# Performance work log

Measured on AMD Instinct MI355X. Metric: run time of the kernel, lower is better.

Reference implementation:

```python
import jax, jax.numpy as jnp
from jax import lax
import numpy as np

K = 7          # kernel size
PAD = 3        # (K-1)//2
KK = K * K     # 49 taps


def setup_inputs() -> dict:
    key = jax.random.key(0)
    ks = jax.random.split(key, 5)
    B, C, H, W = 8, 256, 128, 128
    x = jax.random.normal(ks[0], (B, C, H, W), jnp.float32)
    # conv_offset: Conv2d(2, 3*KK, k=7, pad=3). Small init so offsets are modest.
    w_off = jax.random.normal(ks[1], (3 * KK, 2, K, K), jnp.float32) * 0.01
    b_off = jax.random.normal(ks[2], (3 * KK,), jnp.float32) * 0.01
    # DCN weight: Conv2d(2, 1, k=7)
    w_dcn = jax.random.normal(ks[3], (1, 2, K, K), jnp.float32) * (1.0 / np.sqrt(2 * KK))
    b_dcn = jnp.zeros((1,), jnp.float32)
    bn_gamma = jnp.ones((1,), jnp.float32)
    bn_beta = jnp.zeros((1,), jnp.float32)
    bn_mean = jnp.zeros((1,), jnp.float32)
    bn_var = jnp.ones((1,), jnp.float32)
    return {"x": x, "w_off": w_off, "b_off": b_off, "w_dcn": w_dcn,
            "b_dcn": b_dcn, "bn_gamma": bn_gamma, "bn_beta": bn_beta,
            "bn_mean": bn_mean, "bn_var": bn_var}


def _deform_spatial_att(x, w_off, b_off, w_dcn, b_dcn, bn_gamma, bn_beta, bn_mean, bn_var):
    B, C, H, W = x.shape
    dt = x.dtype
    # channel mean / max pooling -> [B, 2, H, W]
    y = jnp.concatenate([x.mean(1, keepdims=True), x.max(1, keepdims=True)], axis=1)

    # offset/mask generator conv (mmcv ModulatedDeformConv2dPack.conv_offset)
    off = lax.conv_general_dilated(y, w_off, (1, 1), [(PAD, PAD), (PAD, PAD)])
    off = off + b_off[None, :, None, None]                     # [B, 3*KK, H, W]
    o1, o2, m = off[:, :KK], off[:, KK:2 * KK], off[:, 2 * KK:]
    offset = jnp.concatenate([o1, o2], axis=1)                 # [B, 2*KK, H, W]
    dy = offset[:, 0::2]                                       # y-offset per tap, [B, KK, H, W]
    dx = offset[:, 1::2]                                       # x-offset per tap
    mask = jax.nn.sigmoid(m)                                   # modulation, [B, KK, H, W]

    # sampling locations: p = p0 + p_k + offset
    kk = jnp.arange(K, dtype=dt) - PAD
    ky = jnp.repeat(kk, K)                                     # [KK]
    kx = jnp.tile(kk, K)                                       # [KK]
    hh = jnp.arange(H, dtype=dt)
    ww = jnp.arange(W, dtype=dt)
    py = hh[None, None, :, None] + ky[None, :, None, None] + dy   # [B, KK, H, W]
    px = ww[None, None, None, :] + kx[None, :, None, None] + dx

    # bilinear sampling with zero padding outside the feature map
    y0 = jnp.floor(py)
    x0 = jnp.floor(px)
    iy0 = y0.astype(jnp.int32)
    ix0 = x0.astype(jnp.int32)
    iy1 = iy0 + 1
    ix1 = ix0 + 1
    wy1 = py - y0
    wy0 = 1.0 - wy1
    wx1 = px - x0
    wx0 = 1.0 - wx1

    y_flat = y.reshape(B, 2, H * W)

    def gather(iy, ix):
        valid = ((iy >= 0) & (iy < H) & (ix >= 0) & (ix < W))
        idx = jnp.clip(iy, 0, H - 1) * W + jnp.clip(ix, 0, W - 1)   # [B, KK, H, W]
        g = jax.vmap(lambda yb, ib: yb[:, ib])(y_flat, idx)          # [B, 2, KK, H, W]
        return g * valid[:, None].astype(dt)

    val = (gather(iy0, ix0) * (wy0 * wx0)[:, None]
           + gather(iy0, ix1) * (wy0 * wx1)[:, None]
           + gather(iy1, ix0) * (wy1 * wx0)[:, None]
           + gather(iy1, ix1) * (wy1 * wx1)[:, None])                # [B, 2, KK, H, W]

    sampled = val * mask[:, None]
    # deformable conv accumulation: 2 in-channels x 49 taps -> 1 out-channel
    out = jnp.einsum('bckhw,ck->bhw', sampled, w_dcn[0].reshape(2, KK)) + b_dcn
    out = out[:, None]                                               # [B, 1, H, W]

    # BatchNorm2d(1), inference-mode normalization
    eps = 1e-5
    out = (out - bn_mean[None, :, None, None]) * (bn_gamma[None, :, None, None]
          * lax.rsqrt(bn_var[None, :, None, None] + eps)) + bn_beta[None, :, None, None]

    gate = jax.nn.sigmoid(out)                                       # [B, 1, H, W]
    return jnp.broadcast_to(gate, x.shape)


def reference(x, w_off, b_off, w_dcn, b_dcn, bn_gamma, bn_beta, bn_mean, bn_var):
    return _deform_spatial_att(x, w_off, b_off, w_dcn, b_dcn,
                               bn_gamma, bn_beta, bn_mean, bn_var)
```

## Files before the change

kernel.cpp:

```cpp
#include <hip/hip_runtime.h>
#include <cstdint>

#define BB 8
#define CC 256
#define HH 128
#define WW 128
#define HW (HH * WW)

typedef __attribute__((ext_vector_type(8))) short bf16x8;
typedef __attribute__((ext_vector_type(4))) float f32x4;

__device__ __forceinline__ uint32_t f2bf(float f) {
    uint32_t u = __float_as_uint(f);
    return (u + 0x7FFFu + ((u >> 16) & 1u)) >> 16;
}
__device__ __forceinline__ float bf2f(uint32_t u) {
    return __uint_as_float(u << 16);
}

__global__ __launch_bounds__(512) void reduce_meanmax(const float* __restrict__ x,
                                                      float* __restrict__ y2,
                                                      const float* __restrict__ w_off,
                                                      uint16_t* __restrict__ Bpre) {
    const int bh = blockIdx.x;
    const int b  = bh >> 7;
    const int h  = bh & 127;
    const int t  = threadIdx.x;

    if (t < 20) {
        const int idx = bh * 20 + t;
        const int e   = idx & 7;
        const int t1  = idx >> 3;
        const int j   = t1 % 160;
        const int grp = t1 / 160;
        uint16_t v = 0;
        if (grp < 14 && e < 7 && j < 147) {
            const int ci = grp / 7, r = grp % 7;
            const int ch = (j < 49) ? (2 * j) : ((j < 98) ? (2 * (j - 49) + 1) : j);
            v = (uint16_t)f2bf(w_off[(size_t)ch * 98 + ci * 49 + r * 7 + e]);
        }
        Bpre[idx] = v;
    }

    const int wq = t & 31;
    const int cg = t >> 5;
    const float* xb = x + ((size_t)(b * CC + cg * 16) * HH + h) * WW;

    float4 s = make_float4(0.f, 0.f, 0.f, 0.f);
    float4 m = make_float4(-INFINITY, -INFINITY, -INFINITY, -INFINITY);
    #pragma unroll 4
    for (int i = 0; i < 16; ++i) {
        float4 v = ((const float4*)(xb + (size_t)i * HW))[wq];
        s.x += v.x; s.y += v.y; s.z += v.z; s.w += v.w;
        m.x = fmaxf(m.x, v.x); m.y = fmaxf(m.y, v.y);
        m.z = fmaxf(m.z, v.z); m.w = fmaxf(m.w, v.w);
    }

    __shared__ float4 ls[16][32];
    __shared__ float4 lm[16][32];
    ls[cg][wq] = s;
    lm[cg][wq] = m;
    __syncthreads();

    if (t < 32) {
        float4 S = ls[0][t];
        float4 M = lm[0][t];
        #pragma unroll
        for (int g = 1; g < 16; ++g) {
            float4 a = ls[g][t];
            float4 c = lm[g][t];
            S.x += a.x; S.y += a.y; S.z += a.z; S.w += a.w;
            M.x = fmaxf(M.x, c.x); M.y = fmaxf(M.y, c.y);
            M.z = fmaxf(M.z, c.z); M.w = fmaxf(M.w, c.w);
        }
        const float inv = 1.0f / 256.0f;
        float4 o0 = make_float4(S.x * inv, M.x, S.y * inv, M.y);
        float4 o1 = make_float4(S.z * inv, M.z, S.w * inv, M.w);
        float4* yo = (float4*)(y2 + ((size_t)b * HW + (size_t)h * WW) * 2);
        yo[2 * t]     = o0;
        yo[2 * t + 1] = o1;
    }
}

__global__ __launch_bounds__(256) void deform_gate(
    const float* __restrict__ y2, const uint16_t* __restrict__ Bpre,
    const float* __restrict__ b_off,
    const float* __restrict__ w_dcn, const float* __restrict__ b_dcn,
    const float* __restrict__ bn_gamma, const float* __restrict__ bn_beta,
    const float* __restrict__ bn_mean, const float* __restrict__ bn_var,
    float* __restrict__ out)
{
    const int bid  = (blockIdx.x & 7) * 512 + (blockIdx.x >> 3);
    const int rowg = bid >> 2;
    const int qpos = (bid & 3) * 32;
    const int b = rowg >> 7;
    const int h = rowg & 127;
    const int t = threadIdx.x;
    const int wv = t >> 6;
    const int l  = t & 63;
    const int mhalf = wv >> 1;
    const int nhalf = wv & 1;
    const bool act = (l < 49);
    const int ls = act ? l : 0;

    __shared__ uint16_t patch2[16][48];
    __shared__ uint16_t cv[2][16][168];
    __shared__ float gate_blk[32];

    const float2* y2b = (const float2*)y2 + (size_t)b * HW;

    for (int i = t; i < 7 * 40; i += 256) {
        const int r  = i / 40;
        const int xi = i % 40;
        const int xx = qpos + xi - 3;
        const int yy = h + r - 3;
        uint32_t mn = 0, mx = 0;
        if (yy >= 0 && yy < HH && xx >= 0 && xx < WW) {
            float2 g2 = y2b[yy * WW + xx];
            mn = f2bf(g2.x);
            mx = f2bf(g2.y);
        }
        patch2[r][xi]     = (uint16_t)mn;
        patch2[7 + r][xi] = (uint16_t)mx;
    }
    for (int i = t; i < 2 * 48; i += 256)
        patch2[14 + (i / 48)][i % 48] = 0;

    const float b_dy = b_off[2 * ls];
    const float b_dx = b_off[2 * ls + 1];
    const float b_m  = b_off[98 + ls];
    const float wd0 = w_dcn[ls];
    const float wd1 = w_dcn[49 + ls];
    const int kr = ls / 7;
    const int kc = ls % 7;
    const float bscale = bn_gamma[0] * rsqrtf(bn_var[0] + 1e-5f);
    const float gB = (b_dcn[0] - bn_mean[0]) * bscale + bn_beta[0];

    __syncthreads();

    const int m = l & 15;
    const int g = l >> 4;
    const int plocal = mhalf * 16 + m;
    const uint32_t* p32 = (const uint32_t*)&patch2[0][0];

    f32x4 acc[5];
    #pragma unroll
    for (int nn = 0; nn < 5; ++nn) acc[nn] = (f32x4){0.f, 0.f, 0.f, 0.f};

    #pragma unroll
    for (int kt = 0; kt < 4; ++kt) {
        const int grp = kt * 4 + g;
        const int W   = grp * 48 + plocal;
        const uint32_t sh8 = (W & 1) ? 16u : 0u;
        const uint32_t* dp = p32 + (W >> 1);
        const uint32_t d0 = dp[0], d1 = dp[1], d2 = dp[2], d3 = dp[3], d4 = dp[4];
        union { uint32_t u[4]; bf16x8 v; } af;
        af.u[0] = (uint32_t)(((((uint64_t)d1) << 32) | d0) >> sh8);
        af.u[1] = (uint32_t)(((((uint64_t)d2) << 32) | d1) >> sh8);
        af.u[2] = (uint32_t)(((((uint64_t)d3) << 32) | d2) >> sh8);
        af.u[3] = (uint32_t)(((((uint64_t)d4) << 32) | d3) >> sh8);
        #pragma unroll
        for (int nn = 0; nn < 5; ++nn) {
            const int j = (nhalf * 5 + nn) * 16 + m;
            const bf16x8 bfr = *(const bf16x8*)(Bpre + ((grp * 160 + j) << 3));
            acc[nn] = __builtin_amdgcn_mfma_f32_16x16x32_bf16(af.v, bfr, acc[nn], 0, 0, 0);
        }
    }

    #pragma unroll
    for (int nn = 0; nn < 5; ++nn) {
        #pragma unroll
        for (int q = 0; q < 4; ++q) {
            cv[mhalf][g * 4 + q][(nhalf * 5 + nn) * 16 + m] = (uint16_t)f2bf(acc[nn][q]);
        }
    }
    __syncthreads();

    const uint16_t* cvp = &cv[0][0][0];
    #pragma unroll 1
    for (int hb = 0; hb < 2; ++hb) {
        const int p0 = wv * 8 + hb * 4;

        float mkv[4], w00[4], w01[4], w10[4], w11[4];
        float2 g00[4], g01[4], g10[4], g11[4];

        #pragma unroll
        for (int pi = 0; pi < 4; ++pi) {
            const int pp = p0 + pi;
            const int cbase = pp * 168;

            const float dyv = bf2f(cvp[cbase + ls])      + b_dy;
            const float dxv = bf2f(cvp[cbase + 49 + ls]) + b_dx;
            const float mv  = bf2f(cvp[cbase + 98 + ls]) + b_m;
            mkv[pi] = 1.0f / (1.0f + __expf(-mv));

            const float fy = (float)(h + kr - 3) + dyv;
            const float fx = (float)(qpos + pp + kc - 3) + dxv;
            const float fly = floorf(fy), flx = floorf(fx);
            const int iy0 = (int)fly, ix0 = (int)flx;
            const int iy1 = iy0 + 1,  ix1 = ix0 + 1;
            const float wy1 = fy - fly, wy0 = 1.0f - wy1;
            const float wx1 = fx - flx, wx0 = 1.0f - wx1;

            const float vy0 = (iy0 >= 0 && iy0 < HH) ? 1.0f : 0.0f;
            const float vy1 = (iy1 >= 0 && iy1 < HH) ? 1.0f : 0.0f;
            const float vx0 = (ix0 >= 0 && ix0 < WW) ? 1.0f : 0.0f;
            const float vx1 = (ix1 >= 0 && ix1 < WW) ? 1.0f : 0.0f;

            const int cy0 = min(max(iy0, 0), HH - 1) * WW;
            const int cy1 = min(max(iy1, 0), HH - 1) * WW;
            const int cx0 = min(max(ix0, 0), WW - 1);
            const int cx1 = min(max(ix1, 0), WW - 1);

            w00[pi] = wy0 * wx0 * vy0 * vx0;
            w01[pi] = wy0 * wx1 * vy0 * vx1;
            w10[pi] = wy1 * wx0 * vy1 * vx0;
            w11[pi] = wy1 * wx1 * vy1 * vx1;

            g00[pi] = y2b[cy0 + cx0];
            g01[pi] = y2b[cy0 + cx1];
            g10[pi] = y2b[cy1 + cx0];
            g11[pi] = y2b[cy1 + cx1];
        }

        float tv[4];
        #pragma unroll
        for (int pi = 0; pi < 4; ++pi) {
            const float v0s = g00[pi].x * w00[pi] + g01[pi].x * w01[pi]
                            + g10[pi].x * w10[pi] + g11[pi].x * w11[pi];
            const float v1s = g00[pi].y * w00[pi] + g01[pi].y * w01[pi]
                            + g10[pi].y * w10[pi] + g11[pi].y * w11[pi];
            float tval = mkv[pi] * fmaf(v0s, wd0, v1s * wd1);
            tv[pi] = act ? tval : 0.0f;
        }

        #pragma unroll
        for (int off = 1; off < 64; off <<= 1) {
            #pragma unroll
            for (int pi = 0; pi < 4; ++pi)
                tv[pi] += __shfl_xor(tv[pi], off);
        }

        if (l == 0) {
            #pragma unroll
            for (int pi = 0; pi < 4; ++pi) {
                const float o = tv[pi] * bscale + gB;
                gate_blk[p0 + pi] = 1.0f / (1.0f + __expf(-o));
            }
        }
    }

    __syncthreads();

    const size_t ob = (size_t)b * CC * HW + (size_t)h * WW + qpos;
    const f32x4* gb4 = (const f32x4*)gate_blk;
    #pragma unroll
    for (int it = 0; it < 8; ++it) {
        const int idx = it * 256 + t;
        const int c   = idx >> 3;
        const int q4  = idx & 7;
        __builtin_nontemporal_store(gb4[q4], (f32x4*)(out + ob + (size_t)c * HW) + q4);
    }
}

extern "C" void kernel_launch(void* const* d_in, const int* in_sizes, int n_in,
                              void* d_out, int out_size, void* d_ws, size_t ws_size,
                              hipStream_t stream) {
    const float* x        = (const float*)d_in[0];
    const float* w_off    = (const float*)d_in[1];
    const float* b_off    = (const float*)d_in[2];
    const float* w_dcn    = (const float*)d_in[3];
    const float* b_dcn    = (const float*)d_in[4];
    const float* bn_gamma = (const float*)d_in[5];
    const float* bn_beta  = (const float*)d_in[6];
    const float* bn_mean  = (const float*)d_in[7];
    const float* bn_var   = (const float*)d_in[8];
    float* out = (float*)d_out;

    float*    y2   = (float*)d_ws;
    uint16_t* Bpre = (uint16_t*)((char*)d_ws + (1 << 20));

    reduce_meanmax<<<BB * HH, 512, 0, stream>>>(x, y2, w_off, Bpre);
    deform_gate<<<4 * BB * HH, 256, 0, stream>>>(y2, Bpre, b_off, w_dcn, b_dcn,
                                                 bn_gamma, bn_beta, bn_mean, bn_var,
                                                 out);
}
```

Measured before the change: 67.58 us.

## Process a full image row per block in deform_gate instead of quarter rows

Each deform_gate block now handles a whole 128-pixel row with 512 threads (8 waves) instead of 32 pixels with 256 threads. The halo patch covers the full row, which removes redundant halo loads, and each wave runs 10 MFMA accumulators over all output columns. Output stores write full 512-byte row segments per channel. The aim is to cut redundant patch loading and per-block overhead and to make the output writes more contiguous, at the cost of 4x fewer blocks, higher register and LDS use per block, and possibly lower occupancy.

```diff
diff --git a/kernel.cpp b/kernel.cpp
--- a/kernel.cpp
+++ b/kernel.cpp
@@ -82,7 +82,7 @@
     }
 }
 
-__global__ __launch_bounds__(256) void deform_gate(
+__global__ __launch_bounds__(512) void deform_gate(
     const float* __restrict__ y2, const uint16_t* __restrict__ Bpre,
     const float* __restrict__ b_off,
     const float* __restrict__ w_dcn, const float* __restrict__ b_dcn,
@@ -90,41 +90,37 @@
     const float* __restrict__ bn_mean, const float* __restrict__ bn_var,
     float* __restrict__ out)
 {
-    const int bid  = (blockIdx.x & 7) * 512 + (blockIdx.x >> 3);
-    const int rowg = bid >> 2;
-    const int qpos = (bid & 3) * 32;
-    const int b = rowg >> 7;
-    const int h = rowg & 127;
+    const int bid = (blockIdx.x & 7) * 128 + (blockIdx.x >> 3);
+    const int b = bid >> 7;
+    const int h = bid & 127;
     const int t = threadIdx.x;
     const int wv = t >> 6;
     const int l  = t & 63;
-    const int mhalf = wv >> 1;
-    const int nhalf = wv & 1;
     const bool act = (l < 49);
     const int ls = act ? l : 0;
 
-    __shared__ uint16_t patch2[16][48];
-    __shared__ uint16_t cv[2][16][168];
-    __shared__ float gate_blk[32];
+    __shared__ uint16_t patch2[16][144];
+    __shared__ uint16_t cv[128][160];
+    __shared__ float gate_row[128];
 
     const float2* y2b = (const float2*)y2 + (size_t)b * HW;
 
-    for (int i = t; i < 7 * 40; i += 256) {
-        const int r  = i / 40;
-        const int xi = i % 40;
-        const int xx = qpos + xi - 3;
-        const int yy = h + r - 3;
-        uint32_t mn = 0, mx = 0;
-        if (yy >= 0 && yy < HH && xx >= 0 && xx < WW) {
-            float2 g2 = y2b[yy * WW + xx];
-            mn = f2bf(g2.x);
-            mx = f2bf(g2.y);
-        }
-        patch2[r][xi]     = (uint16_t)mn;
-        patch2[7 + r][xi] = (uint16_t)mx;
-    }
-    for (int i = t; i < 2 * 48; i += 256)
-        patch2[14 + (i / 48)][i % 48] = 0;
+    for (int i = t; i < 16 * 144; i += 512) {
+        const int r  = i / 144;
+        const int xi = i % 144;
+        uint16_t v = 0;
+        if (r < 14 && xi < 136) {
+            const int ci = (r >= 7) ? 1 : 0;
+            const int rr = r - 7 * ci;
+            const int xx = xi - 3;
+            const int yy = h + rr - 3;
+            if (yy >= 0 && yy < HH && xx >= 0 && xx < WW) {
+                float2 g2 = y2b[yy * WW + xx];
+                v = (uint16_t)(ci ? f2bf(g2.y) : f2bf(g2.x));
+            }
+        }
+        patch2[r][xi] = v;
+    }
 
     const float b_dy = b_off[2 * ls];
     const float b_dx = b_off[2 * ls + 1];
@@ -140,17 +136,17 @@
 
     const int m = l & 15;
     const int g = l >> 4;
-    const int plocal = mhalf * 16 + m;
+    const int plocal = wv * 16 + m;
     const uint32_t* p32 = (const uint32_t*)&patch2[0][0];
 
-    f32x4 acc[5];
-    #pragma unroll
-    for (int nn = 0; nn < 5; ++nn) acc[nn] = (f32x4){0.f, 0.f, 0.f, 0.f};
+    f32x4 acc[10];
+    #pragma unroll
+    for (int nn = 0; nn < 10; ++nn) acc[nn] = (f32x4){0.f, 0.f, 0.f, 0.f};
 
     #pragma unroll
     for (int kt = 0; kt < 4; ++kt) {
         const int grp = kt * 4 + g;
-        const int W   = grp * 48 + plocal;
+        const int W   = grp * 144 + plocal;
         const uint32_t sh8 = (W & 1) ? 16u : 0u;
         const uint32_t* dp = p32 + (W >> 1);
         const uint32_t d0 = dp[0], d1 = dp[1], d2 = dp[2], d3 = dp[3], d4 = dp[4];
@@ -160,26 +156,26 @@
         af.u[2] = (uint32_t)(((((uint64_t)d3) << 32) | d2) >> sh8);
         af.u[3] = (uint32_t)(((((uint64_t)d4) << 32) | d3) >> sh8);
         #pragma unroll
-        for (int nn = 0; nn < 5; ++nn) {
-            const int j = (nhalf * 5 + nn) * 16 + m;
+        for (int nn = 0; nn < 10; ++nn) {
+            const int j = nn * 16 + m;
             const bf16x8 bfr = *(const bf16x8*)(Bpre + ((grp * 160 + j) << 3));
             acc[nn] = __builtin_amdgcn_mfma_f32_16x16x32_bf16(af.v, bfr, acc[nn], 0, 0, 0);
         }
     }
 
     #pragma unroll
-    for (int nn = 0; nn < 5; ++nn) {
+    for (int nn = 0; nn < 10; ++nn) {
         #pragma unroll
         for (int q = 0; q < 4; ++q) {
-            cv[mhalf][g * 4 + q][(nhalf * 5 + nn) * 16 + m] = (uint16_t)f2bf(acc[nn][q]);
-        }
-    }
-    __syncthreads();
-
-    const uint16_t* cvp = &cv[0][0][0];
+            cv[wv * 16 + g * 4 + q][nn * 16 + m] = (uint16_t)f2bf(acc[nn][q]);
+        }
+    }
+    __syncthreads();
+
+    const uint16_t* cvp = &cv[0][0];
     #pragma unroll 1
-    for (int hb = 0; hb < 2; ++hb) {
-        const int p0 = wv * 8 + hb * 4;
+    for (int hb = 0; hb < 4; ++hb) {
+        const int p0 = wv * 16 + hb * 4;
 
         float mkv[4], w00[4], w01[4], w10[4], w11[4];
         float2 g00[4], g01[4], g10[4], g11[4];
@@ -187,7 +183,7 @@
         #pragma unroll
         for (int pi = 0; pi < 4; ++pi) {
             const int pp = p0 + pi;
-            const int cbase = pp * 168;
+            const int cbase = pp * 160;
 
             const float dyv = bf2f(cvp[cbase + ls])      + b_dy;
             const float dxv = bf2f(cvp[cbase + 49 + ls]) + b_dx;
@@ -195,7 +191,7 @@
             mkv[pi] = 1.0f / (1.0f + __expf(-mv));
 
             const float fy = (float)(h + kr - 3) + dyv;
-            const float fx = (float)(qpos + pp + kc - 3) + dxv;
+            const float fx = (float)(pp + kc - 3) + dxv;
             const float fly = floorf(fy), flx = floorf(fx);
             const int iy0 = (int)fly, ix0 = (int)flx;
             const int iy1 = iy0 + 1,  ix1 = ix0 + 1;
@@ -245,21 +241,21 @@
             #pragma unroll
             for (int pi = 0; pi < 4; ++pi) {
                 const float o = tv[pi] * bscale + gB;
-                gate_blk[p0 + pi] = 1.0f / (1.0f + __expf(-o));
+                gate_row[p0 + pi] = 1.0f / (1.0f + __expf(-o));
             }
         }
     }
 
     __syncthreads();
 
-    const size_t ob = (size_t)b * CC * HW + (size_t)h * WW + qpos;
-    const f32x4* gb4 = (const f32x4*)gate_blk;
-    #pragma unroll
-    for (int it = 0; it < 8; ++it) {
-        const int idx = it * 256 + t;
-        const int c   = idx >> 3;
-        const int q4  = idx & 7;
-        __builtin_nontemporal_store(gb4[q4], (f32x4*)(out + ob + (size_t)c * HW) + q4);
+    const size_t ob = (size_t)b * CC * HW + (size_t)h * WW;
+    const f32x4* gr4 = (const f32x4*)gate_row;
+    #pragma unroll
+    for (int it = 0; it < 16; ++it) {
+        const int idx = it * 512 + t;
+        const int c   = idx >> 5;
+        const int q   = idx & 31;
+        __builtin_nontemporal_store(gr4[q], (f32x4*)(out + ob + (size_t)c * HW) + q);
     }
 }
 
@@ -281,7 +277,7 @@
     uint16_t* Bpre = (uint16_t*)((char*)d_ws + (1 << 20));
 
     reduce_meanmax<<<BB * HH, 512, 0, stream>>>(x, y2, w_off, Bpre);
-    deform_gate<<<4 * BB * HH, 256, 0, stream>>>(y2, Bpre, b_off, w_dcn, b_dcn,
-                                                 bn_gamma, bn_beta, bn_mean, bn_var,
-                                                 out);
-}
+    deform_gate<<<BB * HH, 512, 0, stream>>>(y2, Bpre, b_off, w_dcn, b_dcn,
+                                             bn_gamma, bn_beta, bn_mean, bn_var,
+                                             out);
+}
```

Result: slower. 72.87 us (+7.8%).
